# Kernel tuning notes

Hardware: AMD Instinct MI355X
Metric: run time of the kernel (lower is better)

The kernel has to match this reference:

```python
import jax, jax.numpy as jnp
import numpy as np

B, L, D, H, DK = 2, 1024, 1024, 16, 64
LN_EPS = 1e-5


def setup_inputs() -> dict:
    key = jax.random.key(0)
    ks = jax.random.split(key, 4)
    x = jax.random.normal(ks[0], (B, L, D), dtype=jnp.float32)
    W_qkv = jax.random.normal(ks[1], (D, 3 * D), dtype=jnp.float32) * 0.02
    W_o = jax.random.normal(ks[2], (D, D), dtype=jnp.float32) * 0.02
    W_LTM = jax.random.normal(ks[3], (H, DK, DK), dtype=jnp.float32) * 0.5
    return {
        "x": x,
        "W_qkv": W_qkv,
        "W_o": W_o,
        "W_LTM": W_LTM,
        "V_gs": jnp.zeros((H,), jnp.float32),
        "V_T0": jnp.zeros((H,), jnp.float32),
        "beta_tau": jnp.ones((H,), jnp.float32),
        "beta_gm": jnp.ones((H,), jnp.float32) * 0.1,
        "C_ch": jnp.ones((H,), jnp.float32),
        "gamma": jnp.ones((H,), jnp.float32) * 0.1,
        "alpha_ppd": jnp.ones((1,), jnp.float32),
        "IC_threshold": jnp.ones((1,), jnp.float32),
        "gate": jnp.zeros((H,), jnp.float32),
    }


def _stp_physics(W_LTM, V_gs, V_T0, beta_tau, beta_gm, C_ch, alpha_ppd, IC_threshold):
    # per-head params broadcast to (H, dk, dk)
    V_eff = V_gs[:, None, None] - V_T0[:, None, None] + W_LTM  # U_T = 1.0
    sp = jax.nn.softplus(V_eff)
    g_ch = beta_tau[:, None, None] * sp
    retention = jnp.exp(-g_ch / C_ch[:, None, None])  # = 1 - Lambda
    G = beta_gm[:, None, None] * sp * jax.nn.sigmoid(V_eff)
    sign_mask = jnp.tanh(alpha_ppd * (g_ch - IC_threshold))
    return retention, G, sign_mask


def reference(x, W_qkv, W_o, W_LTM, V_gs, V_T0, beta_tau, beta_gm, C_ch,
              gamma, alpha_ppd, IC_threshold, gate):
    Bb, Ll, Dd = x.shape
    qkv = (x @ W_qkv).reshape(Bb, Ll, 3, H, DK)
    q, k, v = qkv[:, :, 0], qkv[:, :, 1], qkv[:, :, 2]  # (B,L,H,dk)

    # LayerNorm over dk, no affine
    mu = jnp.mean(k, axis=-1, keepdims=True)
    var = jnp.var(k, axis=-1, keepdims=True)
    k_normed = (k - mu) * jax.lax.rsqrt(var + LN_EPS)

    # ---- causal softmax attention ----
    scale = 1.0 / np.sqrt(DK)
    attn = jnp.einsum('bihd,bjhd->bhij', q, k) * scale
    causal = jnp.tril(jnp.ones((Ll, Ll), dtype=bool))
    attn = jnp.where(causal[None, None], attn, -jnp.inf)
    attn = jax.nn.softmax(attn, axis=-1)
    softmax_out = jnp.einsum('bhij,bjhd->bihd', attn, v)  # (B,L,H,dk)

    # ---- STP fast-weight recurrence ----
    retention, G, sign_mask = _stp_physics(W_LTM, V_gs, V_T0, beta_tau,
                                           beta_gm, C_ch, alpha_ppd, IC_threshold)
    coeff = gamma[:, None, None] * sign_mask * G  # (H,dk,dk)

    def step(F_state, qkv_t):
        q_t, k_t, v_t = qkv_t  # (B,H,dk) each; k_t is normed
        hebbian = jnp.einsum('bhd,bhe->bhde', v_t, k_t)
        F_new = retention[None] * F_state + coeff[None] * hebbian
        y_t = jnp.einsum('bhde,bhe->bhd', W_LTM[None] + F_new, q_t)
        return F_new, y_t

    xs = (jnp.moveaxis(q, 1, 0), jnp.moveaxis(k_normed, 1, 0), jnp.moveaxis(v, 1, 0))
    F0 = jnp.zeros((Bb, H, DK, DK), dtype=x.dtype)
    _, ys = jax.lax.scan(step, F0, xs)
    stp_out = jnp.moveaxis(ys, 0, 1)  # (B,L,H,dk)

    g = jax.nn.sigmoid(gate)[None, None, :, None]
    y = g * softmax_out + (1.0 - g) * stp_out
    y = y.reshape(Bb, Ll, Dd)
    return y @ W_o
```

## Files before the change

### kernel.cpp

```cpp
#include <hip/hip_runtime.h>
#include <hip/hip_bf16.h>
#include <math.h>

#define LQ 1024
#define DH 1024
#define NH 16
#define DKH 64

typedef __bf16 bf16x8 __attribute__((ext_vector_type(8)));
typedef float f32x4 __attribute__((ext_vector_type(4)));
typedef const unsigned int __attribute__((address_space(1)))* gas1_t;
typedef unsigned int __attribute__((address_space(3)))* las3_t;

__device__ __forceinline__ unsigned pack2bf(float a, float b) {
  union { __hip_bfloat16 h[2]; unsigned u; } t;
  t.h[0] = __float2bfloat16(a);
  t.h[1] = __float2bfloat16(b);
  return t.u;
}
__device__ __forceinline__ unsigned short bfbits(float x) {
  __hip_bfloat16 h = __float2bfloat16(x);
  return *(unsigned short*)&h;
}
__device__ __forceinline__ void bf4w(float* dst, uint2 r) {
  dst[0] = __uint_as_float(r.x << 16);
  dst[1] = __uint_as_float(r.x & 0xffff0000u);
  dst[2] = __uint_as_float(r.y << 16);
  dst[3] = __uint_as_float(r.y & 0xffff0000u);
}

__global__ __launch_bounds__(256) void prep_kernel(
    const float* __restrict__ x, const float* __restrict__ W_qkv, const float* __restrict__ W_o,
    const float* __restrict__ W_LTM, const float* __restrict__ V_gs, const float* __restrict__ V_T0,
    const float* __restrict__ beta_tau, const float* __restrict__ beta_gm, const float* __restrict__ C_ch,
    const float* __restrict__ gamma_, const float* __restrict__ alpha_ppd, const float* __restrict__ IC_thr,
    const float* __restrict__ gate,
    __hip_bfloat16* __restrict__ xb, __hip_bfloat16* __restrict__ wqt, __hip_bfloat16* __restrict__ wot,
    float* __restrict__ ret, float* __restrict__ ret64, float* __restrict__ co, float* __restrict__ g_out) {
  __shared__ float ts[32][33];
  const int bx = blockIdx.x, tid = threadIdx.x;
  if (bx < 256) {
    int idx = bx * 256 + tid;
    int h = idx >> 12;
    float w = W_LTM[idx];
    float veff = V_gs[h] - V_T0[h] + w;
    float sp = fmaxf(veff, 0.f) + log1pf(expf(-fabsf(veff)));
    float gch = beta_tau[h] * sp;
    float e1 = gch / C_ch[h];
    float sig = 1.f / (1.f + expf(-veff));
    float G = beta_gm[h] * sp * sig;
    float sm = tanhf(alpha_ppd[0] * (gch - IC_thr[0]));
    ret[idx] = expf(-e1);
    ret64[idx] = expf(-64.f * e1);
    co[idx] = gamma_[h] * sm * G;
    if (idx < NH) g_out[idx] = 1.f / (1.f + expf(-gate[idx]));
  } else if (bx < 2304) {
    size_t i = (size_t)((bx - 256) * 256 + tid) * 4;
    float4 v = *(const float4*)(x + i);
    __hip_bfloat16 t[4] = {__float2bfloat16(v.x), __float2bfloat16(v.y),
                           __float2bfloat16(v.z), __float2bfloat16(v.w)};
    *(uint2*)(xb + i) = *(uint2*)t;
  } else {
    const float* W;
    __hip_bfloat16* Wt;
    int n0, k0, N;
    if (bx < 5376) {
      int idx = bx - 2304;
      W = W_qkv; Wt = wqt; N = 3072;
      n0 = (idx % 96) * 32; k0 = (idx / 96) * 32;
    } else {
      int idx = bx - 5376;
      W = W_o; Wt = wot; N = 1024;
      n0 = (idx & 31) * 32; k0 = (idx >> 5) * 32;
    }
    int r = tid >> 5, c = tid & 31;
#pragma unroll
    for (int i = 0; i < 4; i++) ts[r + 8 * i][c] = W[(size_t)(k0 + r + 8 * i) * N + n0 + c];
    __syncthreads();
#pragma unroll
    for (int i = 0; i < 4; i++)
      Wt[(size_t)(n0 + r + 8 * i) * 1024 + k0 + c] = __float2bfloat16(ts[c][r + 8 * i]);
  }
}

__global__ __launch_bounds__(256) void gemm_qkv_kernel(
    const __hip_bfloat16* __restrict__ A, const __hip_bfloat16* __restrict__ Bt,
    __hip_bfloat16* __restrict__ C, __hip_bfloat16* __restrict__ knb,
    __hip_bfloat16* __restrict__ vt, int M, int N, int K) {
  __shared__ union {
    struct { unsigned short As[128 * 32]; unsigned short Bs[128 * 32]; } ab;
    unsigned short Vt[4][64][68];
  } sm;
  const int tid = threadIdx.x;
  const int w = tid >> 6, lane = tid & 63;
  const int quad = lane >> 4, l16 = lane & 15;
  const int wm = w & 1, wn = w >> 1;
  const int row0 = blockIdx.y * 128, col0 = blockIdx.x * 128;
  const int sr = lane >> 2;
  const int sk = (lane & 3) * 8;
  f32x4 acc[4][4];
#pragma unroll
  for (int i = 0; i < 4; i++)
#pragma unroll
    for (int j = 0; j < 4; j++) acc[i][j] = (f32x4){0.f, 0.f, 0.f, 0.f};

  for (int k0 = 0; k0 < K; k0 += 32) {
    __syncthreads();
#pragma unroll
    for (int c = 0; c < 2; c++) {
      int s = c * 4 + w;
      const __hip_bfloat16* gA = A + (size_t)(row0 + s * 16 + sr) * K + k0 + sk;
      __builtin_amdgcn_global_load_lds((gas1_t)gA, (las3_t)((char*)sm.ab.As + s * 1024), 16, 0, 0);
      const __hip_bfloat16* gB = Bt + (size_t)(col0 + s * 16 + sr) * K + k0 + sk;
      __builtin_amdgcn_global_load_lds((gas1_t)gB, (las3_t)((char*)sm.ab.Bs + s * 1024), 16, 0, 0);
    }
    __syncthreads();
    bf16x8 af[4], bfr[4];
#pragma unroll
    for (int i = 0; i < 4; i++)
      af[i] = *(const bf16x8*)((const char*)sm.ab.As + (((wm * 64 + i * 16 + l16) * 32 + quad * 8) << 1));
#pragma unroll
    for (int j = 0; j < 4; j++)
      bfr[j] = *(const bf16x8*)((const char*)sm.ab.Bs + (((wn * 64 + j * 16 + l16) * 32 + quad * 8) << 1));
#pragma unroll
    for (int i = 0; i < 4; i++)
#pragma unroll
      for (int j = 0; j < 4; j++)
        acc[i][j] = __builtin_amdgcn_mfma_f32_16x16x32_bf16(af[i], bfr[j], acc[i][j], 0, 0, 0);
  }
#pragma unroll
  for (int i = 0; i < 4; i++) {
    int rowb = row0 + wm * 64 + i * 16 + quad * 4;
#pragma unroll
    for (int j = 0; j < 4; j++) {
      int col = col0 + wn * 64 + j * 16 + l16;
#pragma unroll
      for (int r = 0; r < 4; r++)
        C[(size_t)(rowb + r) * N + col] = __float2bfloat16(acc[i][j][r]);
    }
  }
  const int sec = col0 >> 10;
  if (sec == 1) {
    const int hh = ((col0 & 1023) >> 6) + wn;
#pragma unroll
    for (int i = 0; i < 4; i++) {
      f32x4 s1 = {0.f, 0.f, 0.f, 0.f}, s2 = {0.f, 0.f, 0.f, 0.f};
#pragma unroll
      for (int j = 0; j < 4; j++)
#pragma unroll
        for (int r = 0; r < 4; r++) {
          s1[r] += acc[i][j][r];
          s2[r] += acc[i][j][r] * acc[i][j][r];
        }
#pragma unroll
      for (int m = 1; m <= 8; m <<= 1)
#pragma unroll
        for (int r = 0; r < 4; r++) {
          s1[r] += __shfl_xor(s1[r], m);
          s2[r] += __shfl_xor(s2[r], m);
        }
#pragma unroll
      for (int r = 0; r < 4; r++) {
        float mu = s1[r] * (1.f / 64.f);
        float var = s2[r] * (1.f / 64.f) - mu * mu;
        float inv = rsqrtf(var + 1e-5f);
        int row = row0 + wm * 64 + i * 16 + quad * 4 + r;
#pragma unroll
        for (int j = 0; j < 4; j++)
          knb[((size_t)row * NH + hh) * DKH + j * 16 + l16] = __float2bfloat16((acc[i][j][r] - mu) * inv);
      }
    }
  } else if (sec == 2) {
    __syncthreads();
    const int hh = ((col0 & 1023) >> 6) + wn;
#pragma unroll
    for (int i = 0; i < 4; i++)
#pragma unroll
      for (int j = 0; j < 4; j++)
#pragma unroll
        for (int r = 0; r < 4; r++)
          sm.Vt[w][j * 16 + l16][i * 16 + quad * 4 + r] = bfbits(acc[i][j][r]);
    const int b = row0 >> 10;
    const int t0 = (row0 & 1023) + wm * 64;
    const int bh = b * NH + hh;
    const int cc = lane & 7, ddl = lane >> 3;
#pragma unroll
    for (int pass = 0; pass < 8; pass++) {
      int d = pass * 8 + ddl;
      uint2 a0 = *(const uint2*)&sm.Vt[w][d][cc * 8];
      uint2 a1 = *(const uint2*)&sm.Vt[w][d][cc * 8 + 4];
      uint4 val = {a0.x, a0.y, a1.x, a1.y};
      *(uint4*)(vt + ((size_t)bh * DKH + d) * LQ + t0 + cc * 8) = val;
    }
  }
}

__global__ __launch_bounds__(256) void gemm_bt64_kernel(
    const __hip_bfloat16* __restrict__ A, const __hip_bfloat16* __restrict__ Bt,
    float* __restrict__ C, int M, int N, int K) {
  __shared__ unsigned short As[64 * 32];
  __shared__ unsigned short Bs[64 * 32];
  const int tid = threadIdx.x;
  const int w = tid >> 6, lane = tid & 63;
  const int quad = lane >> 4, l16 = lane & 15;
  const int wm = w & 1, wn = w >> 1;
  const int row0 = blockIdx.y * 64, col0 = blockIdx.x * 64;
  const int sr = lane >> 2;
  const int sk = (lane & 3) * 8;
  f32x4 acc[2][2];
#pragma unroll
  for (int i = 0; i < 2; i++)
#pragma unroll
    for (int j = 0; j < 2; j++) acc[i][j] = (f32x4){0.f, 0.f, 0.f, 0.f};

  for (int k0 = 0; k0 < K; k0 += 32) {
    __syncthreads();
    const __hip_bfloat16* gA = A + (size_t)(row0 + w * 16 + sr) * K + k0 + sk;
    __builtin_amdgcn_global_load_lds((gas1_t)gA, (las3_t)((char*)As + w * 1024), 16, 0, 0);
    const __hip_bfloat16* gB = Bt + (size_t)(col0 + w * 16 + sr) * K + k0 + sk;
    __builtin_amdgcn_global_load_lds((gas1_t)gB, (las3_t)((char*)Bs + w * 1024), 16, 0, 0);
    __syncthreads();
    bf16x8 af[2], bfr[2];
#pragma unroll
    for (int i = 0; i < 2; i++)
      af[i] = *(const bf16x8*)((const char*)As + (((wm * 32 + i * 16 + l16) * 32 + quad * 8) << 1));
#pragma unroll
    for (int j = 0; j < 2; j++)
      bfr[j] = *(const bf16x8*)((const char*)Bs + (((wn * 32 + j * 16 + l16) * 32 + quad * 8) << 1));
#pragma unroll
    for (int i = 0; i < 2; i++)
#pragma unroll
      for (int j = 0; j < 2; j++)
        acc[i][j] = __builtin_amdgcn_mfma_f32_16x16x32_bf16(af[i], bfr[j], acc[i][j], 0, 0, 0);
  }
#pragma unroll
  for (int i = 0; i < 2; i++) {
    int rowb = row0 + wm * 32 + i * 16 + quad * 4;
#pragma unroll
    for (int j = 0; j < 2; j++) {
      int col = col0 + wn * 32 + j * 16 + l16;
#pragma unroll
      for (int r = 0; r < 4; r++)
        C[(size_t)(rowb + r) * N + col] = acc[i][j][r];
    }
  }
}

__global__ __launch_bounds__(256) void attn_mfma_kernel(
    const __hip_bfloat16* __restrict__ qkvb, const __hip_bfloat16* __restrict__ vt,
    __hip_bfloat16* __restrict__ sob) {
  const int it = 15 - blockIdx.x;
  const int h = blockIdx.y, b = blockIdx.z;
  const int bh = b * NH + h;
  const int tid = threadIdx.x;
  const int w = tid >> 6, lane = tid & 63;
  const int l16 = lane & 15, quad = lane >> 4;
  __shared__ __attribute__((aligned(16))) __hip_bfloat16 Ks[8 * 64 * 8];
  __shared__ __attribute__((aligned(16))) __hip_bfloat16 Vs[8 * 64 * 8];
  const int i0 = it * 64;
  const int q_abs = i0 + w * 16 + l16;
  bf16x8 aq[2];
  aq[0] = *(const bf16x8*)(qkvb + (size_t)(b * LQ + q_abs) * 3 * DH + h * DKH + quad * 8);
  aq[1] = *(const bf16x8*)(qkvb + (size_t)(b * LQ + q_abs) * 3 * DH + h * DKH + 32 + quad * 8);
  f32x4 o[4];
#pragma unroll
  for (int dt = 0; dt < 4; dt++) o[dt] = (f32x4){0.f, 0.f, 0.f, 0.f};
  float mrun = -3e38f, lrun = 0.f;

  for (int jt = 0; jt <= it; jt++) {
    const int j0 = jt * 64;
    __syncthreads();
#pragma unroll
    for (int ff = 0; ff < 2; ff++) {
      const int f = w * 2 + ff;
      const int nt = f >> 1, kk = f & 1;
      const __hip_bfloat16* gk = qkvb + (size_t)(b * LQ + j0 + nt * 16 + l16) * 3 * DH + DH +
                                 h * DKH + kk * 32 + quad * 8;
      __builtin_amdgcn_global_load_lds((gas1_t)gk, (las3_t)(Ks + f * 512), 16, 0, 0);
      const __hip_bfloat16* gv = vt + ((size_t)bh * DKH + nt * 16 + l16) * LQ + j0 + kk * 32 + quad * 8;
      __builtin_amdgcn_global_load_lds((gas1_t)gv, (las3_t)(Vs + f * 512), 16, 0, 0);
    }
    __syncthreads();
    f32x4 s[4];
#pragma unroll
    for (int nt = 0; nt < 4; nt++) s[nt] = (f32x4){0.f, 0.f, 0.f, 0.f};
#pragma unroll
    for (int kk = 0; kk < 2; kk++)
#pragma unroll
      for (int nt = 0; nt < 4; nt++) {
        bf16x8 bk = *(const bf16x8*)(Ks + ((nt * 2 + kk) * 64 + lane) * 8);
        s[nt] = __builtin_amdgcn_mfma_f32_16x16x32_bf16(bk, aq[kk], s[nt], 0, 0, 0);
      }
#pragma unroll
    for (int nt = 0; nt < 4; nt++)
#pragma unroll
      for (int r = 0; r < 4; r++) {
        float sv = s[nt][r] * 0.125f;
        if (jt == it && (j0 + nt * 16 + quad * 4 + r > q_abs)) sv = -1e30f;
        s[nt][r] = sv;
      }
    float mx = -3e38f;
#pragma unroll
    for (int nt = 0; nt < 4; nt++)
#pragma unroll
      for (int r = 0; r < 4; r++) mx = fmaxf(mx, s[nt][r]);
    mx = fmaxf(mx, __shfl_xor(mx, 16));
    mx = fmaxf(mx, __shfl_xor(mx, 32));
    float mn = fmaxf(mrun, mx);
    float al = __expf(mrun - mn);
    mrun = mn;
    float p[4][4];
    float rs = 0.f;
#pragma unroll
    for (int nt = 0; nt < 4; nt++)
#pragma unroll
      for (int r = 0; r < 4; r++) {
        float pv = __expf(s[nt][r] - mn);
        p[nt][r] = pv;
        rs += pv;
      }
    rs += __shfl_xor(rs, 16);
    rs += __shfl_xor(rs, 32);
    lrun = lrun * al + rs;
    unsigned pk[4][2];
#pragma unroll
    for (int nt = 0; nt < 4; nt++) {
      pk[nt][0] = pack2bf(p[nt][0], p[nt][1]);
      pk[nt][1] = pack2bf(p[nt][2], p[nt][3]);
    }
    const int srcA = l16 | ((quad & 1) << 5);
    const bool hi_sel = (quad >> 1) != 0;
    bf16x8 ap[2];
#pragma unroll
    for (int kk = 0; kk < 2; kk++) {
      union { unsigned u[4]; bf16x8 v; } cv;
#pragma unroll
      for (int g = 0; g < 2; g++) {
        int src = srcA + (g << 4);
        unsigned lo0 = (unsigned)__shfl((int)pk[kk * 2][0], src);
        unsigned lo1 = (unsigned)__shfl((int)pk[kk * 2][1], src);
        unsigned hi0 = (unsigned)__shfl((int)pk[kk * 2 + 1][0], src);
        unsigned hi1 = (unsigned)__shfl((int)pk[kk * 2 + 1][1], src);
        cv.u[g * 2] = hi_sel ? hi0 : lo0;
        cv.u[g * 2 + 1] = hi_sel ? hi1 : lo1;
      }
      ap[kk] = cv.v;
    }
#pragma unroll
    for (int dt = 0; dt < 4; dt++)
#pragma unroll
      for (int r = 0; r < 4; r++) o[dt][r] *= al;
#pragma unroll
    for (int kk = 0; kk < 2; kk++)
#pragma unroll
      for (int dt = 0; dt < 4; dt++) {
        bf16x8 bv = *(const bf16x8*)(Vs + ((dt * 2 + kk) * 64 + lane) * 8);
        o[dt] = __builtin_amdgcn_mfma_f32_16x16x32_bf16(bv, ap[kk], o[dt], 0, 0, 0);
      }
  }
  float inv = 1.f / lrun;
  __hip_bfloat16* ob = sob + ((size_t)(b * LQ + q_abs) * NH + h) * DKH + quad * 4;
#pragma unroll
  for (int dt = 0; dt < 4; dt++) {
    uint2 val = {pack2bf(o[dt][0] * inv, o[dt][1] * inv),
                 pack2bf(o[dt][2] * inv, o[dt][3] * inv)};
    *(uint2*)(ob + dt * 16) = val;
  }
}

__global__ __launch_bounds__(256) void state_kernel(
    const __hip_bfloat16* __restrict__ qkvb, const __hip_bfloat16* __restrict__ knb,
    const float* __restrict__ ret_g, const float* __restrict__ co_g, float* __restrict__ S) {
  const int bh = blockIdx.x >> 1;
  const int half = blockIdx.x & 1;
  const int c = blockIdx.y;
  const int bb = bh >> 4, h = bh & 15;
  const int tid = threadIdx.x;
  const int dl = tid >> 3, j = tid & 7;
  const int d = half * 32 + dl;
  float F[8], R[8], Cc[8];
  const int base = h * 4096 + d * 64 + j * 8;
#pragma unroll
  for (int i = 0; i < 8; i++) {
    F[i] = 0.f;
    R[i] = ret_g[base + i];
    Cc[i] = co_g[base + i];
  }
  __shared__ float kb[2][8][64], vb[2][8][64];
  const int t00 = c * 64;
  const int sten = tid >> 7;
  const int sli = tid & 127;
  const int ss = sli >> 4;
  const int se = (sli & 15) * 4;
  {
    int t = t00 + ss;
    uint2 raw = (sten == 0)
        ? *(const uint2*)(knb + ((size_t)(bb * LQ + t) * NH + h) * DKH + se)
        : *(const uint2*)(qkvb + ((size_t)(bb * LQ + t) * 3 + 2) * DH + h * DKH + se);
    bf4w(sten == 0 ? &kb[0][ss][se] : &vb[0][ss][se], raw);
  }
  __syncthreads();
  for (int sc = 0; sc < 8; sc++) {
    const int p = sc & 1;
    uint2 raw;
    if (sc < 7) {
      int t = t00 + (sc + 1) * 8 + ss;
      raw = (sten == 0)
          ? *(const uint2*)(knb + ((size_t)(bb * LQ + t) * NH + h) * DKH + se)
          : *(const uint2*)(qkvb + ((size_t)(bb * LQ + t) * 3 + 2) * DH + h * DKH + se);
    }
#pragma unroll
    for (int s = 0; s < 8; s++) {
      float vd = vb[p][s][d];
      float4 k0 = *(const float4*)&kb[p][s][j * 8];
      float4 k1 = *(const float4*)&kb[p][s][j * 8 + 4];
      float ke[8] = {k0.x, k0.y, k0.z, k0.w, k1.x, k1.y, k1.z, k1.w};
#pragma unroll
      for (int i = 0; i < 8; i++) F[i] = fmaf(Cc[i] * vd, ke[i], R[i] * F[i]);
    }
    if (sc < 7) bf4w(sten == 0 ? &kb[p ^ 1][ss][se] : &vb[p ^ 1][ss][se], raw);
    __syncthreads();
  }
  const size_t sb = ((size_t)c * 2048 + ((size_t)bb * 16 + h) * 64 + d) * 64 + j * 8;
#pragma unroll
  for (int i = 0; i < 8; i++) S[sb + i] = F[i];
}

__global__ __launch_bounds__(256) void combine_kernel(
    const float* __restrict__ S, const float* __restrict__ ret64, float* __restrict__ Fs) {
  int n = blockIdx.x * 256 + threadIdx.x;
  float r64 = ret64[n & 65535];
  float F = 0.f;
  Fs[n] = 0.f;
#pragma unroll
  for (int c = 1; c < 16; c++) {
    F = fmaf(r64, F, S[(size_t)(c - 1) * 131072 + n]);
    Fs[(size_t)c * 131072 + n] = F;
  }
}

__global__ __launch_bounds__(256) void scan_out_kernel(
    const __hip_bfloat16* __restrict__ qkvb, const __hip_bfloat16* __restrict__ knb,
    const float* __restrict__ W_LTM, const float* __restrict__ ret_g, const float* __restrict__ co_g,
    const float* __restrict__ Fs, const __hip_bfloat16* __restrict__ sob,
    const float* __restrict__ g, __hip_bfloat16* __restrict__ mixb) {
  const int bh = blockIdx.x >> 1;
  const int half = blockIdx.x & 1;
  const int c = blockIdx.y;
  const int bb = bh >> 4, h = bh & 15;
  const int tid = threadIdx.x;
  const int dl = tid >> 3, j = tid & 7;
  const int d = half * 32 + dl;
  const float gh = g[h];
  float F[8], R[8], Cc[8], W[8];
  const int base = h * 4096 + d * 64 + j * 8;
  const size_t nbase = (size_t)c * 131072 + (((size_t)bb * 16 + h) * 64 + d) * 64 + j * 8;
#pragma unroll
  for (int i = 0; i < 8; i++) {
    F[i] = Fs[nbase + i];
    R[i] = ret_g[base + i];
    Cc[i] = co_g[base + i];
    W[i] = W_LTM[base + i];
  }
  __shared__ float qb[2][8][64], kb[2][8][64], vb[2][8][64];
  const int t00 = c * 64;
  const int sten = tid >> 7;
  const int sli = tid & 127;
  const int ss = sli >> 4;
  const int se = (sli & 15) * 4;
  const int vs = tid >> 5;
  const int ve = (tid & 31) * 2;
  {
    int t = t00 + ss, tv = t00 + vs;
    uint2 rqk = (sten == 0)
        ? *(const uint2*)(qkvb + (size_t)(bb * LQ + t) * 3 * DH + h * DKH + se)
        : *(const uint2*)(knb + ((size_t)(bb * LQ + t) * NH + h) * DKH + se);
    unsigned rv = *(const unsigned*)(qkvb + ((size_t)(bb * LQ + tv) * 3 + 2) * DH + h * DKH + ve);
    bf4w(sten == 0 ? &qb[0][ss][se] : &kb[0][ss][se], rqk);
    vb[0][vs][ve] = __uint_as_float(rv << 16);
    vb[0][vs][ve + 1] = __uint_as_float(rv & 0xffff0000u);
  }
  __syncthreads();
  for (int sc = 0; sc < 8; sc++) {
    const int p = sc & 1;
    uint2 rqk;
    unsigned rv;
    if (sc < 7) {
      int t = t00 + (sc + 1) * 8 + ss, tv = t00 + (sc + 1) * 8 + vs;
      rqk = (sten == 0)
          ? *(const uint2*)(qkvb + (size_t)(bb * LQ + t) * 3 * DH + h * DKH + se)
          : *(const uint2*)(knb + ((size_t)(bb * LQ + t) * NH + h) * DKH + se);
      rv = *(const unsigned*)(qkvb + ((size_t)(bb * LQ + tv) * 3 + 2) * DH + h * DKH + ve);
    }
    float ykeep = 0.f;
#pragma unroll
    for (int s = 0; s < 8; s++) {
      float vd = vb[p][s][d];
      float4 k0 = *(const float4*)&kb[p][s][j * 8];
      float4 k1 = *(const float4*)&kb[p][s][j * 8 + 4];
      float4 q0 = *(const float4*)&qb[p][s][j * 8];
      float4 q1 = *(const float4*)&qb[p][s][j * 8 + 4];
      float ke[8] = {k0.x, k0.y, k0.z, k0.w, k1.x, k1.y, k1.z, k1.w};
      float qe[8] = {q0.x, q0.y, q0.z, q0.w, q1.x, q1.y, q1.z, q1.w};
      float yp = 0.f;
#pragma unroll
      for (int i = 0; i < 8; i++) {
        F[i] = fmaf(Cc[i] * vd, ke[i], R[i] * F[i]);
        yp = fmaf(W[i] + F[i], qe[i], yp);
      }
      yp += __shfl_xor(yp, 1);
      yp += __shfl_xor(yp, 2);
      yp += __shfl_xor(yp, 4);
      if (j == s) ykeep = yp;
    }
    {
      const size_t oi = ((size_t)(bb * LQ + t00 + sc * 8 + j) * NH + h) * DKH + d;
      float sv = __bfloat162float(sob[oi]);
      mixb[oi] = __float2bfloat16(gh * sv + (1.f - gh) * ykeep);
    }
    if (sc < 7) {
      bf4w(sten == 0 ? &qb[p ^ 1][ss][se] : &kb[p ^ 1][ss][se], rqk);
      vb[p ^ 1][vs][ve] = __uint_as_float(rv << 16);
      vb[p ^ 1][vs][ve + 1] = __uint_as_float(rv & 0xffff0000u);
    }
    __syncthreads();
  }
}

extern "C" void kernel_launch(void* const* d_in, const int* in_sizes, int n_in,
                              void* d_out, int out_size, void* d_ws, size_t ws_size,
                              hipStream_t stream) {
  (void)in_sizes; (void)n_in; (void)out_size; (void)ws_size;
  const float* x        = (const float*)d_in[0];
  const float* W_qkv    = (const float*)d_in[1];
  const float* W_o      = (const float*)d_in[2];
  const float* W_LTM    = (const float*)d_in[3];
  const float* V_gs     = (const float*)d_in[4];
  const float* V_T0     = (const float*)d_in[5];
  const float* beta_tau = (const float*)d_in[6];
  const float* beta_gm  = (const float*)d_in[7];
  const float* C_ch     = (const float*)d_in[8];
  const float* gamma_   = (const float*)d_in[9];
  const float* alpha_p  = (const float*)d_in[10];
  const float* IC_thr   = (const float*)d_in[11];
  const float* gate     = (const float*)d_in[12];

  float* ws  = (float*)d_ws;
  __hip_bfloat16* qkvb = (__hip_bfloat16*)ws;
  __hip_bfloat16* knb  = (__hip_bfloat16*)(ws + 3145728);
  __hip_bfloat16* sob  = (__hip_bfloat16*)(ws + 4194304);
  __hip_bfloat16* mixb = (__hip_bfloat16*)(ws + 5242880);
  __hip_bfloat16* vtb  = (__hip_bfloat16*)(ws + 6291456);
  __hip_bfloat16* xb   = (__hip_bfloat16*)(ws + 7340032);
  __hip_bfloat16* wqt  = (__hip_bfloat16*)(ws + 8388608);
  __hip_bfloat16* wot  = (__hip_bfloat16*)(ws + 9961472);
  float* ret   = ws + 10485760;
  float* ret64 = ret + 65536;
  float* co    = ret64 + 65536;
  float* g     = co + 65536;
  float* Sbuf  = g + 64;
  float* Fs    = Sbuf + 1966080;
  float* out = (float*)d_out;

  prep_kernel<<<6400, 256, 0, stream>>>(x, W_qkv, W_o, W_LTM, V_gs, V_T0, beta_tau, beta_gm,
                                        C_ch, gamma_, alpha_p, IC_thr, gate,
                                        xb, wqt, wot, ret, ret64, co, g);
  gemm_qkv_kernel<<<dim3(24, 16), 256, 0, stream>>>(xb, wqt, qkvb, knb, vtb, 2048, 3072, 1024);
  attn_mfma_kernel<<<dim3(16, 16, 2), 256, 0, stream>>>(qkvb, vtb, sob);
  state_kernel<<<dim3(64, 15), 256, 0, stream>>>(qkvb, knb, ret, co, Sbuf);
  combine_kernel<<<512, 256, 0, stream>>>(Sbuf, ret64, Fs);
  scan_out_kernel<<<dim3(64, 16), 256, 0, stream>>>(qkvb, knb, W_LTM, ret, co, Fs, sob, g, mixb);
  gemm_bt64_kernel<<<dim3(16, 32), 256, 0, stream>>>(mixb, wot, out, 2048, 1024, 1024);
}
```

Baseline: 214.9 us.

## Halve QKV GEMM row tile and deepen output GEMM K-step to 64

The QKV projection GEMM now uses 64x128 tiles instead of 128x128, doubling the grid to 768 blocks for better CU occupancy and balance, with the V-transpose epilogue adjusted to match. The output projection GEMM now stages a K-slice of 64 per barrier pair, using a fragment-ordered LDS layout so each lane reads its MFMA operand contiguously. This halves the number of synchronizations in the output GEMM. The trade-off is less operand reuse per block in the QKV GEMM.

```diff
diff --git a/kernel.cpp b/kernel.cpp
--- a/kernel.cpp
+++ b/kernel.cpp
@@ -88,49 +88,51 @@
     __hip_bfloat16* __restrict__ C, __hip_bfloat16* __restrict__ knb,
     __hip_bfloat16* __restrict__ vt, int M, int N, int K) {
   __shared__ union {
-    struct { unsigned short As[128 * 32]; unsigned short Bs[128 * 32]; } ab;
-    unsigned short Vt[4][64][68];
+    struct { unsigned short As[64 * 32]; unsigned short Bs[128 * 32]; } ab;
+    unsigned short Vt[4][64][36];
   } sm;
   const int tid = threadIdx.x;
   const int w = tid >> 6, lane = tid & 63;
   const int quad = lane >> 4, l16 = lane & 15;
   const int wm = w & 1, wn = w >> 1;
-  const int row0 = blockIdx.y * 128, col0 = blockIdx.x * 128;
+  const int row0 = blockIdx.y * 64, col0 = blockIdx.x * 128;
   const int sr = lane >> 2;
   const int sk = (lane & 3) * 8;
-  f32x4 acc[4][4];
-#pragma unroll
-  for (int i = 0; i < 4; i++)
+  f32x4 acc[2][4];
+#pragma unroll
+  for (int i = 0; i < 2; i++)
 #pragma unroll
     for (int j = 0; j < 4; j++) acc[i][j] = (f32x4){0.f, 0.f, 0.f, 0.f};
 
   for (int k0 = 0; k0 < K; k0 += 32) {
     __syncthreads();
-#pragma unroll
-    for (int c = 0; c < 2; c++) {
-      int s = c * 4 + w;
-      const __hip_bfloat16* gA = A + (size_t)(row0 + s * 16 + sr) * K + k0 + sk;
-      __builtin_amdgcn_global_load_lds((gas1_t)gA, (las3_t)((char*)sm.ab.As + s * 1024), 16, 0, 0);
-      const __hip_bfloat16* gB = Bt + (size_t)(col0 + s * 16 + sr) * K + k0 + sk;
-      __builtin_amdgcn_global_load_lds((gas1_t)gB, (las3_t)((char*)sm.ab.Bs + s * 1024), 16, 0, 0);
-    }
-    __syncthreads();
-    bf16x8 af[4], bfr[4];
-#pragma unroll
-    for (int i = 0; i < 4; i++)
-      af[i] = *(const bf16x8*)((const char*)sm.ab.As + (((wm * 64 + i * 16 + l16) * 32 + quad * 8) << 1));
+    {
+      const __hip_bfloat16* gA = A + (size_t)(row0 + w * 16 + sr) * K + k0 + sk;
+      __builtin_amdgcn_global_load_lds((gas1_t)gA, (las3_t)((char*)sm.ab.As + w * 1024), 16, 0, 0);
+#pragma unroll
+      for (int c = 0; c < 2; c++) {
+        int s = c * 4 + w;
+        const __hip_bfloat16* gB = Bt + (size_t)(col0 + s * 16 + sr) * K + k0 + sk;
+        __builtin_amdgcn_global_load_lds((gas1_t)gB, (las3_t)((char*)sm.ab.Bs + s * 1024), 16, 0, 0);
+      }
+    }
+    __syncthreads();
+    bf16x8 af[2], bfr[4];
+#pragma unroll
+    for (int i = 0; i < 2; i++)
+      af[i] = *(const bf16x8*)((const char*)sm.ab.As + (((wm * 32 + i * 16 + l16) * 32 + quad * 8) << 1));
 #pragma unroll
     for (int j = 0; j < 4; j++)
       bfr[j] = *(const bf16x8*)((const char*)sm.ab.Bs + (((wn * 64 + j * 16 + l16) * 32 + quad * 8) << 1));
 #pragma unroll
-    for (int i = 0; i < 4; i++)
+    for (int i = 0; i < 2; i++)
 #pragma unroll
       for (int j = 0; j < 4; j++)
         acc[i][j] = __builtin_amdgcn_mfma_f32_16x16x32_bf16(af[i], bfr[j], acc[i][j], 0, 0, 0);
   }
 #pragma unroll
-  for (int i = 0; i < 4; i++) {
-    int rowb = row0 + wm * 64 + i * 16 + quad * 4;
+  for (int i = 0; i < 2; i++) {
+    int rowb = row0 + wm * 32 + i * 16 + quad * 4;
 #pragma unroll
     for (int j = 0; j < 4; j++) {
       int col = col0 + wn * 64 + j * 16 + l16;
@@ -140,10 +142,10 @@
     }
   }
   const int sec = col0 >> 10;
+  const int hh = ((col0 & 1023) >> 6) + wn;
   if (sec == 1) {
-    const int hh = ((col0 & 1023) >> 6) + wn;
-#pragma unroll
-    for (int i = 0; i < 4; i++) {
+#pragma unroll
+    for (int i = 0; i < 2; i++) {
       f32x4 s1 = {0.f, 0.f, 0.f, 0.f}, s2 = {0.f, 0.f, 0.f, 0.f};
 #pragma unroll
       for (int j = 0; j < 4; j++)
@@ -164,7 +166,7 @@
         float mu = s1[r] * (1.f / 64.f);
         float var = s2[r] * (1.f / 64.f) - mu * mu;
         float inv = rsqrtf(var + 1e-5f);
-        int row = row0 + wm * 64 + i * 16 + quad * 4 + r;
+        int row = row0 + wm * 32 + i * 16 + quad * 4 + r;
 #pragma unroll
         for (int j = 0; j < 4; j++)
           knb[((size_t)row * NH + hh) * DKH + j * 16 + l16] = __float2bfloat16((acc[i][j][r] - mu) * inv);
@@ -172,21 +174,20 @@
     }
   } else if (sec == 2) {
     __syncthreads();
-    const int hh = ((col0 & 1023) >> 6) + wn;
-#pragma unroll
-    for (int i = 0; i < 4; i++)
+#pragma unroll
+    for (int i = 0; i < 2; i++)
 #pragma unroll
       for (int j = 0; j < 4; j++)
 #pragma unroll
         for (int r = 0; r < 4; r++)
           sm.Vt[w][j * 16 + l16][i * 16 + quad * 4 + r] = bfbits(acc[i][j][r]);
     const int b = row0 >> 10;
-    const int t0 = (row0 & 1023) + wm * 64;
+    const int t0 = (row0 & 1023) + wm * 32;
     const int bh = b * NH + hh;
-    const int cc = lane & 7, ddl = lane >> 3;
-#pragma unroll
-    for (int pass = 0; pass < 8; pass++) {
-      int d = pass * 8 + ddl;
+    const int cc = lane & 3, ddl = lane >> 2;
+#pragma unroll
+    for (int pass = 0; pass < 4; pass++) {
+      int d = pass * 16 + ddl;
       uint2 a0 = *(const uint2*)&sm.Vt[w][d][cc * 8];
       uint2 a1 = *(const uint2*)&sm.Vt[w][d][cc * 8 + 4];
       uint4 val = {a0.x, a0.y, a1.x, a1.y};
@@ -195,43 +196,50 @@
   }
 }
 
-__global__ __launch_bounds__(256) void gemm_bt64_kernel(
+__global__ __launch_bounds__(256) void gemm_out_kernel(
     const __hip_bfloat16* __restrict__ A, const __hip_bfloat16* __restrict__ Bt,
     float* __restrict__ C, int M, int N, int K) {
-  __shared__ unsigned short As[64 * 32];
-  __shared__ unsigned short Bs[64 * 32];
+  __shared__ unsigned short As[8 * 512];
+  __shared__ unsigned short Bs[8 * 512];
   const int tid = threadIdx.x;
   const int w = tid >> 6, lane = tid & 63;
   const int quad = lane >> 4, l16 = lane & 15;
   const int wm = w & 1, wn = w >> 1;
   const int row0 = blockIdx.y * 64, col0 = blockIdx.x * 64;
-  const int sr = lane >> 2;
-  const int sk = (lane & 3) * 8;
+  const int fr = lane & 15;
+  const int fk = (lane >> 4) * 8;
   f32x4 acc[2][2];
 #pragma unroll
   for (int i = 0; i < 2; i++)
 #pragma unroll
     for (int j = 0; j < 2; j++) acc[i][j] = (f32x4){0.f, 0.f, 0.f, 0.f};
 
-  for (int k0 = 0; k0 < K; k0 += 32) {
-    __syncthreads();
-    const __hip_bfloat16* gA = A + (size_t)(row0 + w * 16 + sr) * K + k0 + sk;
-    __builtin_amdgcn_global_load_lds((gas1_t)gA, (las3_t)((char*)As + w * 1024), 16, 0, 0);
-    const __hip_bfloat16* gB = Bt + (size_t)(col0 + w * 16 + sr) * K + k0 + sk;
-    __builtin_amdgcn_global_load_lds((gas1_t)gB, (las3_t)((char*)Bs + w * 1024), 16, 0, 0);
-    __syncthreads();
-    bf16x8 af[2], bfr[2];
-#pragma unroll
-    for (int i = 0; i < 2; i++)
-      af[i] = *(const bf16x8*)((const char*)As + (((wm * 32 + i * 16 + l16) * 32 + quad * 8) << 1));
-#pragma unroll
-    for (int j = 0; j < 2; j++)
-      bfr[j] = *(const bf16x8*)((const char*)Bs + (((wn * 32 + j * 16 + l16) * 32 + quad * 8) << 1));
-#pragma unroll
-    for (int i = 0; i < 2; i++)
+  for (int k0 = 0; k0 < K; k0 += 64) {
+    __syncthreads();
+#pragma unroll
+    for (int kk = 0; kk < 2; kk++) {
+      const int f = kk * 4 + w;
+      const __hip_bfloat16* gA = A + (size_t)(row0 + w * 16 + fr) * K + k0 + kk * 32 + fk;
+      __builtin_amdgcn_global_load_lds((gas1_t)gA, (las3_t)((char*)As + f * 1024), 16, 0, 0);
+      const __hip_bfloat16* gB = Bt + (size_t)(col0 + w * 16 + fr) * K + k0 + kk * 32 + fk;
+      __builtin_amdgcn_global_load_lds((gas1_t)gB, (las3_t)((char*)Bs + f * 1024), 16, 0, 0);
+    }
+    __syncthreads();
+#pragma unroll
+    for (int kk = 0; kk < 2; kk++) {
+      bf16x8 af[2], bfr[2];
+#pragma unroll
+      for (int i = 0; i < 2; i++)
+        af[i] = *(const bf16x8*)((const char*)As + (((kk * 4 + wm * 2 + i) * 64 + lane) << 4));
 #pragma unroll
       for (int j = 0; j < 2; j++)
-        acc[i][j] = __builtin_amdgcn_mfma_f32_16x16x32_bf16(af[i], bfr[j], acc[i][j], 0, 0, 0);
+        bfr[j] = *(const bf16x8*)((const char*)Bs + (((kk * 4 + wn * 2 + j) * 64 + lane) << 4));
+#pragma unroll
+      for (int i = 0; i < 2; i++)
+#pragma unroll
+        for (int j = 0; j < 2; j++)
+          acc[i][j] = __builtin_amdgcn_mfma_f32_16x16x32_bf16(af[i], bfr[j], acc[i][j], 0, 0, 0);
+    }
   }
 #pragma unroll
   for (int i = 0; i < 2; i++) {
@@ -565,10 +573,10 @@
   prep_kernel<<<6400, 256, 0, stream>>>(x, W_qkv, W_o, W_LTM, V_gs, V_T0, beta_tau, beta_gm,
                                         C_ch, gamma_, alpha_p, IC_thr, gate,
                                         xb, wqt, wot, ret, ret64, co, g);
-  gemm_qkv_kernel<<<dim3(24, 16), 256, 0, stream>>>(xb, wqt, qkvb, knb, vtb, 2048, 3072, 1024);
+  gemm_qkv_kernel<<<dim3(24, 32), 256, 0, stream>>>(xb, wqt, qkvb, knb, vtb, 2048, 3072, 1024);
   attn_mfma_kernel<<<dim3(16, 16, 2), 256, 0, stream>>>(qkvb, vtb, sob);
   state_kernel<<<dim3(64, 15), 256, 0, stream>>>(qkvb, knb, ret, co, Sbuf);
   combine_kernel<<<512, 256, 0, stream>>>(Sbuf, ret64, Fs);
   scan_out_kernel<<<dim3(64, 16), 256, 0, stream>>>(qkvb, knb, W_LTM, ret, co, Fs, sob, g, mixb);
-  gemm_bt64_kernel<<<dim3(16, 32), 256, 0, stream>>>(mixb, wot, out, 2048, 1024, 1024);
-}
+  gemm_out_kernel<<<dim3(16, 32), 256, 0, stream>>>(mixb, wot, out, 2048, 1024, 1024);
+}
```

Measured after the change: 208.3 us. -3.1%, faster.
